# Performance work log

Measured on AMD Instinct MI355X. Metric: run time of the kernel, lower is better.

Reference implementation:

```python
import jax, jax.numpy as jnp
import numpy as np

HID = 512
HEADS = 8
HEAD_DIM = HID // HEADS
BS, SEQ = 4, 2048


def setup_inputs() -> dict:
    key = jax.random.key(0)
    ks = jax.random.split(key, 12)
    s = 0.02
    return {
        "query": jax.random.normal(ks[0], (BS, SEQ, HID), jnp.float32),
        "key": jax.random.normal(ks[1], (BS, SEQ, HID), jnp.float32),
        "value": jax.random.normal(ks[2], (BS, SEQ, HID), jnp.float32),
        "query_mask": jnp.ones((BS, SEQ), dtype=bool),
        "key_mask": jnp.ones((BS, SEQ), dtype=bool),
        "Wq": jax.random.normal(ks[3], (HID, HID), jnp.float32) * s,
        "bq": jnp.zeros((HID,), jnp.float32),
        "Wk": jax.random.normal(ks[4], (HID, HID), jnp.float32) * s,
        "bk": jnp.zeros((HID,), jnp.float32),
        "Wv": jax.random.normal(ks[5], (HID, HID), jnp.float32) * s,
        "bv": jnp.zeros((HID,), jnp.float32),
        "Wo": jax.random.normal(ks[6], (HID, HID), jnp.float32) * s,
        "bo": jnp.zeros((HID,), jnp.float32),
    }


def _mha(query, key, value, query_mask, key_mask, Wq, bq, Wk, bk, Wv, bv, Wo, bo):
    bs, q_len, _ = query.shape
    k_len = key.shape[1]
    scale = jnp.sqrt(jnp.asarray(HEAD_DIM, query.dtype))

    def proj(x, W, b):  # nn.Linear: x @ W^T + b, then split heads -> [b,h,s,d]
        y = jnp.einsum('bse,fe->bsf', x, W) + b
        return y.reshape(bs, -1, HEADS, HEAD_DIM).transpose(0, 2, 1, 3)

    q = proj(query, Wq, bq)
    k = proj(key, Wk, bk)
    v = proj(value, Wv, bv)

    energy = jnp.einsum('bhqd,bhkd->bhqk', q, k) / scale  # [b,h,q,k]
    neg = -jnp.finfo(energy.dtype).max

    pad_mask = query_mask[:, None, :, None] & key_mask[:, None, None, :]
    energy = jnp.where(pad_mask, energy, neg)

    # causal: mask positions where q_idx < k_idx
    causal = jnp.arange(q_len)[:, None] < jnp.arange(k_len)[None, :]
    energy = jnp.where(causal[None, None], neg, energy)

    attn = jax.nn.softmax(energy, axis=-1)  # dropout p=0.0 -> identity
    x = jnp.einsum('bhqk,bhkd->bhqd', attn, v)
    x = x.transpose(0, 2, 1, 3).reshape(bs, q_len, HID)
    return jnp.einsum('bse,fe->bsf', x, Wo) + bo


def reference(query, key, value, query_mask, key_mask, Wq, bq, Wk, bk, Wv, bv, Wo, bo):
    return _mha(query, key, value, query_mask, key_mask, Wq, bq, Wk, bk, Wv, bv, Wo, bo)
```

## Files before the change

kernel.cpp:

```cpp
#include <hip/hip_runtime.h>
#include <hip/hip_bf16.h>

#define DEVI __device__ __forceinline__

typedef __attribute__((ext_vector_type(4)))  float f32x4;
typedef __attribute__((ext_vector_type(16))) float f32x16;
typedef __attribute__((ext_vector_type(8)))  short bf16x8;

constexpr int BS    = 4;
constexpr int SEQ   = 2048;
constexpr int HID   = 512;
constexpr int HEADS = 8;
constexpr int HD    = 64;
constexpr int M     = BS * SEQ;

constexpr float QSCALE = 0.125f * 1.4426950408889634f;

DEVI ushort f2bf(float f) {
    union { float f; unsigned u; } a; a.f = f;
    unsigned r = a.u + 0x7fffu + ((a.u >> 16) & 1u);
    return (ushort)(r >> 16);
}

DEVI f32x4 mfma16(bf16x8 a, bf16x8 b, f32x4 c) {
    return __builtin_amdgcn_mfma_f32_16x16x32_bf16(a, b, c, 0, 0, 0);
}
DEVI f32x16 mfma32(bf16x8 a, bf16x8 b, f32x16 c) {
    return __builtin_amdgcn_mfma_f32_32x32x16_bf16(a, b, c, 0, 0, 0);
}

DEVI void gl_lds16(const ushort* g, ushort* l) {
    __builtin_amdgcn_global_load_lds(
        (const __attribute__((address_space(1))) void*)g,
        (__attribute__((address_space(3))) void*)l,
        16, 0, 0);
}

DEVI unsigned cvtpk(float lo, float hi) {
    unsigned r;
    asm("v_cvt_pk_bf16_f32 %0, %1, %2" : "=v"(r) : "v"(lo), "v"(hi));
    return r;
}

__global__ void cast_all(const float* __restrict__ q, const float* __restrict__ k,
                         const float* __restrict__ v,
                         const float* __restrict__ wq, const float* __restrict__ wk,
                         const float* __restrict__ wv, const float* __restrict__ wo,
                         ushort* __restrict__ oq, ushort* __restrict__ ok,
                         ushort* __restrict__ ov,
                         ushort* __restrict__ owq, ushort* __restrict__ owk,
                         ushort* __restrict__ owv, ushort* __restrict__ owo)
{
    const size_t NQ4 = (size_t)M * HID / 4;
    const size_t NW4 = (size_t)HID * HID / 4;
    const size_t total = 3 * NQ4 + 4 * NW4;
    for (size_t i = (size_t)blockIdx.x * blockDim.x + threadIdx.x; i < total;
         i += (size_t)gridDim.x * blockDim.x) {
        const float* src; ushort* dst; size_t j;
        if (i < 3 * NQ4) {
            size_t a = i / NQ4; j = i - a * NQ4;
            src = (a == 0) ? q : (a == 1) ? k : v;
            dst = (a == 0) ? oq : (a == 1) ? ok : ov;
        } else {
            size_t t = i - 3 * NQ4;
            size_t a = t / NW4; j = t - a * NW4;
            src = (a == 0) ? wq : (a == 1) ? wk : (a == 2) ? wv : wo;
            dst = (a == 0) ? owq : (a == 1) ? owk : (a == 2) ? owv : owo;
        }
        float4 f = ((const float4*)src)[j];
        ushort4 u;
        u.x = f2bf(f.x); u.y = f2bf(f.y); u.z = f2bf(f.z); u.w = f2bf(f.w);
        ((ushort4*)dst)[j] = u;
    }
}

DEVI void gemm_core(const ushort* __restrict__ A, const ushort* __restrict__ W,
                    const float* __restrict__ bias, void* __restrict__ out,
                    float scale, int mode, ushort* lA, ushort* lB)
{
    constexpr int BK = 32;
    const int tid  = threadIdx.x;
    const int lane = tid & 63, w = tid >> 6;
    const int wm = w >> 1, wn = w & 1;
    const int l15 = lane & 15, lg = lane >> 4;
    const int m0 = blockIdx.x * 64, n0 = blockIdx.y * 128;
    const int srow = tid >> 2, sc8 = (tid & 3) * 8;

    f32x4 acc[2][4];
    #pragma unroll
    for (int i = 0; i < 2; i++)
        #pragma unroll
        for (int n = 0; n < 4; n++) acc[i][n] = f32x4{0.f, 0.f, 0.f, 0.f};

    for (int k0 = 0; k0 < HID; k0 += BK) {
        gl_lds16(A + (size_t)(m0 + srow) * HID + k0 + sc8, lA + w * 512);
        gl_lds16(W + (size_t)(n0 + srow) * HID + k0 + sc8, lB + w * 512);
        gl_lds16(W + (size_t)(n0 + 64 + srow) * HID + k0 + sc8, lB + 2048 + w * 512);
        __syncthreads();

        bf16x8 af[2], bfr[4];
        #pragma unroll
        for (int i = 0; i < 2; i++)
            af[i] = *(const bf16x8*)(lA + (wm * 32 + i * 16 + l15) * BK + lg * 8);
        #pragma unroll
        for (int n = 0; n < 4; n++)
            bfr[n] = *(const bf16x8*)(lB + (wn * 64 + n * 16 + l15) * BK + lg * 8);
        #pragma unroll
        for (int i = 0; i < 2; i++)
            #pragma unroll
            for (int n = 0; n < 4; n++)
                acc[i][n] = mfma16(af[i], bfr[n], acc[i][n]);
        __syncthreads();
    }

    #pragma unroll
    for (int i = 0; i < 2; i++) {
        #pragma unroll
        for (int n = 0; n < 4; n++) {
            const int col = n0 + wn * 64 + n * 16 + l15;
            const float bb = bias[col];
            const int rbase = m0 + wm * 32 + i * 16 + lg * 4;
            #pragma unroll
            for (int jj = 0; jj < 4; jj++) {
                float v = (acc[i][n][jj] + bb) * scale;
                const int r = rbase + jj;
                if (mode == 3) {
                    ((float*)out)[(size_t)r * HID + col] = v;
                } else {
                    const int b = r >> 11, s = r & (SEQ - 1);
                    const int h = col >> 6, d = col & 63;
                    const int bh = b * HEADS + h;
                    const int t = s >> 5;
                    const ushort u = f2bf(v);
                    if (mode == 0) {
                        const int l31r = s & 31;
                        const int ds = d >> 4, hif = (d >> 3) & 1, jf = d & 7;
                        ((ushort*)out)[(((size_t)bh * 64 + t) * 4 + ds) * 512 +
                                       (hif * 32 + l31r) * 8 + jf] = u;
                    } else {
                        const int c = s & 31;
                        const int kvh = (c >> 4) & 1, hif = (c >> 2) & 1;
                        const int jf = (c & 3) + ((c >> 3) & 1) * 4;
                        const int dt = d >> 5, drow = d & 31;
                        ((ushort*)out)[(((size_t)bh * 64 + t) * 4 + dt * 2 + kvh) * 512 +
                                       (hif * 32 + drow) * 8 + jf] = u;
                    }
                }
            }
        }
    }
}

__global__ __launch_bounds__(256)
void gemm_qkv(const ushort* __restrict__ Xq, const ushort* __restrict__ Xk,
              const ushort* __restrict__ Xv,
              const ushort* __restrict__ Wq, const ushort* __restrict__ Wk,
              const ushort* __restrict__ Wv,
              const float* __restrict__ bq, const float* __restrict__ bk,
              const float* __restrict__ bv,
              ushort* __restrict__ Qf, ushort* __restrict__ Kf,
              ushort* __restrict__ Vf)
{
    __shared__ ushort lA[64 * 32];
    __shared__ ushort lB[128 * 32];
    const int z = blockIdx.z;
    const ushort* A = z == 0 ? Xq : z == 1 ? Xk : Xv;
    const ushort* W = z == 0 ? Wq : z == 1 ? Wk : Wv;
    const float* bias = z == 0 ? bq : z == 1 ? bk : bv;
    void* out = z == 0 ? (void*)Qf : z == 1 ? (void*)Kf : (void*)Vf;
    gemm_core(A, W, bias, out, z == 0 ? QSCALE : 1.0f, z == 2 ? 2 : 0, lA, lB);
}

__global__ __launch_bounds__(256)
void gemm_o(const ushort* __restrict__ ctx, const ushort* __restrict__ Wo,
            const float* __restrict__ bo, float* __restrict__ out)
{
    __shared__ ushort lA[64 * 32];
    __shared__ ushort lB[128 * 32];
    gemm_core(ctx, Wo, bo, out, 1.0f, 3, lA, lB);
}

__global__ __launch_bounds__(256)
void attn4(const ushort* __restrict__ Qf, const ushort* __restrict__ Kf,
           const ushort* __restrict__ Vf, ushort* __restrict__ ctx)
{
    __shared__ float part[4][2][16][64];
    __shared__ float pml[4][2][32];

    const int tid  = threadIdx.x;
    const int lane = tid & 63, w = tid >> 6;
    const int l31 = lane & 31, hi = lane >> 5;

    const int bid = blockIdx.x;
    const int bh  = bid & 31;
    const int qt  = 63 - (bid >> 5);
    const int qb  = qt * 32;

    const ushort* Qb = Qf + ((size_t)bh * 64 + qt) * 2048;
    const ushort* Kb = Kf + (size_t)bh * 64 * 2048;
    const ushort* Vb = Vf + (size_t)bh * 64 * 2048;

    bf16x8 qf[4];
    #pragma unroll
    for (int ds = 0; ds < 4; ds++)
        qf[ds] = *(const bf16x8*)(Qb + ds * 512 + lane * 8);

    f32x16 acc0 = {}, acc1 = {};
    float mrun = -3e38f, lrun = 0.f;

    bf16x8 kf[4] = {};
    if (w <= qt) {
        const ushort* kp = Kb + (size_t)w * 2048 + lane * 8;
        #pragma unroll
        for (int ds = 0; ds < 4; ds++)
            kf[ds] = *(const bf16x8*)(kp + ds * 512);
    }

    for (int t = w; t <= qt; t += 4) {
        const ushort* vp = Vb + (size_t)t * 2048 + lane * 8;
        const bf16x8 va00 = *(const bf16x8*)(vp);
        const bf16x8 va01 = *(const bf16x8*)(vp + 512);
        const bf16x8 va10 = *(const bf16x8*)(vp + 1024);
        const bf16x8 va11 = *(const bf16x8*)(vp + 1536);

        f32x16 s = {};
        #pragma unroll
        for (int ds = 0; ds < 4; ds++)
            s = mfma32(kf[ds], qf[ds], s);

        {
            const int tn = (t + 4 <= qt) ? t + 4 : t;
            const ushort* kp = Kb + (size_t)tn * 2048 + lane * 8;
            #pragma unroll
            for (int ds = 0; ds < 4; ds++)
                kf[ds] = *(const bf16x8*)(kp + ds * 512);
        }

        if (t == qt) {
            #pragma unroll
            for (int r = 0; r < 16; r++) {
                const int kvrow = (r & 3) + 8 * (r >> 2) + 4 * hi;
                s[r] = (kvrow > l31) ? -3e38f : s[r];
            }
        }

        float m8[8];
        #pragma unroll
        for (int r = 0; r < 8; r++) m8[r] = fmaxf(s[r], s[r + 8]);
        float m4a = fmaxf(m8[0], m8[1]), m4b = fmaxf(m8[2], m8[3]);
        float m4c = fmaxf(m8[4], m8[5]), m4d = fmaxf(m8[6], m8[7]);
        float pmax = fmaxf(fmaxf(m4a, m4b), fmaxf(m4c, m4d));
        pmax = fmaxf(pmax, __shfl_xor(pmax, 32));

        if (!__all(pmax <= mrun + 8.f)) {
            const float mnew = fmaxf(mrun, pmax);
            const float corr = __builtin_amdgcn_exp2f(mrun - mnew);
            lrun *= corr;
            #pragma unroll
            for (int r = 0; r < 16; r++) { acc0[r] *= corr; acc1[r] *= corr; }
            mrun = mnew;
        }

        float e[16];
        #pragma unroll
        for (int r = 0; r < 16; r++)
            e[r] = __builtin_amdgcn_exp2f(s[r] - mrun);
        float es0 = (e[0] + e[1]) + (e[2] + e[3]);
        float es1 = (e[4] + e[5]) + (e[6] + e[7]);
        float es2 = (e[8] + e[9]) + (e[10] + e[11]);
        float es3 = (e[12] + e[13]) + (e[14] + e[15]);
        float esum = (es0 + es1) + (es2 + es3);
        lrun += esum + __shfl_xor(esum, 32);

        union { unsigned u[4]; bf16x8 v; } pb0, pb1;
        pb0.u[0] = cvtpk(e[0],  e[1]);  pb0.u[1] = cvtpk(e[2],  e[3]);
        pb0.u[2] = cvtpk(e[4],  e[5]);  pb0.u[3] = cvtpk(e[6],  e[7]);
        pb1.u[0] = cvtpk(e[8],  e[9]);  pb1.u[1] = cvtpk(e[10], e[11]);
        pb1.u[2] = cvtpk(e[12], e[13]); pb1.u[3] = cvtpk(e[14], e[15]);

        acc0 = mfma32(va00, pb0.v, acc0);
        acc0 = mfma32(va01, pb1.v, acc0);
        acc1 = mfma32(va10, pb0.v, acc1);
        acc1 = mfma32(va11, pb1.v, acc1);
    }

    #pragma unroll
    for (int r = 0; r < 16; r++) {
        part[w][0][r][lane] = acc0[r];
        part[w][1][r][lane] = acc1[r];
    }
    if (hi == 0) { pml[w][0][l31] = mrun; pml[w][1][l31] = lrun; }
    __syncthreads();

    const float mm0 = pml[0][0][l31], ll0 = pml[0][1][l31];
    const float mm1 = pml[1][0][l31], ll1 = pml[1][1][l31];
    const float mm2 = pml[2][0][l31], ll2 = pml[2][1][l31];
    const float mm3 = pml[3][0][l31], ll3 = pml[3][1][l31];
    const float mstar = fmaxf(fmaxf(mm0, mm1), fmaxf(mm2, mm3));
    const float f0 = __builtin_amdgcn_exp2f(mm0 - mstar);
    const float f1 = __builtin_amdgcn_exp2f(mm1 - mstar);
    const float f2 = __builtin_amdgcn_exp2f(mm2 - mstar);
    const float f3 = __builtin_amdgcn_exp2f(mm3 - mstar);
    const float lstar = ll0 * f0 + ll1 * f1 + ll2 * f2 + ll3 * f3;
    const float inv = 1.f / lstar;

    const int b = bh >> 3, h = bh & 7;
    ushort* op = ctx + ((size_t)(b * SEQ + qb + l31)) * HID + h * HD;
    #pragma unroll
    for (int a = 0; a < 2; a++) {
        float v[4];
        #pragma unroll
        for (int j = 0; j < 4; j++) {
            const int r = 4 * w + j;
            v[j] = (part[0][a][r][lane] * f0 + part[1][a][r][lane] * f1 +
                    part[2][a][r][lane] * f2 + part[3][a][r][lane] * f3) * inv;
        }
        ushort4 o;
        o.x = f2bf(v[0]); o.y = f2bf(v[1]); o.z = f2bf(v[2]); o.w = f2bf(v[3]);
        *(ushort4*)(op + a * 32 + 8 * w + 4 * hi) = o;
    }
}

extern "C" void kernel_launch(void* const* d_in, const int* in_sizes, int n_in,
                              void* d_out, int out_size, void* d_ws, size_t ws_size,
                              hipStream_t stream) {
    const float* q  = (const float*)d_in[0];
    const float* k  = (const float*)d_in[1];
    const float* v  = (const float*)d_in[2];
    const float* Wq = (const float*)d_in[5];
    const float* bq = (const float*)d_in[6];
    const float* Wk = (const float*)d_in[7];
    const float* bk = (const float*)d_in[8];
    const float* Wv = (const float*)d_in[9];
    const float* bv = (const float*)d_in[10];
    const float* Wo = (const float*)d_in[11];
    const float* bo = (const float*)d_in[12];

    char* ws = (char*)d_ws;
    constexpr size_t XSZ = (size_t)M * HID * 2;
    constexpr size_t WSZ = (size_t)HID * HID * 2;
    ushort* Xq  = (ushort*)(ws);
    ushort* Xk  = (ushort*)(ws + XSZ);
    ushort* Xv  = (ushort*)(ws + 2 * XSZ);
    ushort* Wqb = (ushort*)(ws + 3 * XSZ);
    ushort* Wkb = (ushort*)(ws + 3 * XSZ + WSZ);
    ushort* Wvb = (ushort*)(ws + 3 * XSZ + 2 * WSZ);
    ushort* Wob = (ushort*)(ws + 3 * XSZ + 3 * WSZ);
    ushort* Qf  = (ushort*)(ws + 3 * XSZ + 4 * WSZ);
    ushort* Kf  = (ushort*)(ws + 4 * XSZ + 4 * WSZ);
    ushort* Vf  = (ushort*)(ws + 5 * XSZ + 4 * WSZ);
    ushort* ctx = (ushort*)(ws + 6 * XSZ + 4 * WSZ);

    cast_all<<<2048, 256, 0, stream>>>(q, k, v, Wq, Wk, Wv, Wo,
                                       Xq, Xk, Xv, Wqb, Wkb, Wvb, Wob);

    dim3 gqkv(M / 64, HID / 128, 3);
    gemm_qkv<<<gqkv, 256, 0, stream>>>(Xq, Xk, Xv, Wqb, Wkb, Wvb,
                                       bq, bk, bv, Qf, Kf, Vf);

    attn4<<<BS * HEADS * (SEQ / 32), 256, 0, stream>>>(Qf, Kf, Vf, ctx);

    dim3 go(M / 64, HID / 128);
    gemm_o<<<go, 256, 0, stream>>>(ctx, Wob, bo, (float*)d_out);
}
```

Before: 95.82 us.

## Fuse activation bf16 cast into QKV GEMM, enlarge M tile, prefetch V

The separate cast of the query/key/value activations is removed: the QKV GEMM now loads fp32 rows directly, converts them to bf16 in registers and writes them to LDS, so only the weights are cast up front. Both GEMMs move from 64x128 to 128x128 tiles, which doubles the accumulators per wave and halves the grid. The attention loop now prefetches the next tile's V fragments together with K into registers. This saves a full round trip of activations through global memory, at the cost of higher register pressure, fewer blocks and a synchronous fp32 load path in the GEMM.

```diff
diff --git a/kernel.cpp b/kernel.cpp
--- a/kernel.cpp
+++ b/kernel.cpp
@@ -42,39 +42,24 @@
     return r;
 }
 
-__global__ void cast_all(const float* __restrict__ q, const float* __restrict__ k,
-                         const float* __restrict__ v,
-                         const float* __restrict__ wq, const float* __restrict__ wk,
-                         const float* __restrict__ wv, const float* __restrict__ wo,
-                         ushort* __restrict__ oq, ushort* __restrict__ ok,
-                         ushort* __restrict__ ov,
-                         ushort* __restrict__ owq, ushort* __restrict__ owk,
-                         ushort* __restrict__ owv, ushort* __restrict__ owo)
-{
-    const size_t NQ4 = (size_t)M * HID / 4;
-    const size_t NW4 = (size_t)HID * HID / 4;
-    const size_t total = 3 * NQ4 + 4 * NW4;
-    for (size_t i = (size_t)blockIdx.x * blockDim.x + threadIdx.x; i < total;
-         i += (size_t)gridDim.x * blockDim.x) {
-        const float* src; ushort* dst; size_t j;
-        if (i < 3 * NQ4) {
-            size_t a = i / NQ4; j = i - a * NQ4;
-            src = (a == 0) ? q : (a == 1) ? k : v;
-            dst = (a == 0) ? oq : (a == 1) ? ok : ov;
-        } else {
-            size_t t = i - 3 * NQ4;
-            size_t a = t / NW4; j = t - a * NW4;
-            src = (a == 0) ? wq : (a == 1) ? wk : (a == 2) ? wv : wo;
-            dst = (a == 0) ? owq : (a == 1) ? owk : (a == 2) ? owv : owo;
-        }
-        float4 f = ((const float4*)src)[j];
-        ushort4 u;
-        u.x = f2bf(f.x); u.y = f2bf(f.y); u.z = f2bf(f.z); u.w = f2bf(f.w);
-        ((ushort4*)dst)[j] = u;
-    }
-}
-
-DEVI void gemm_core(const ushort* __restrict__ A, const ushort* __restrict__ W,
+__global__ void cast_w(const float* __restrict__ wq, const float* __restrict__ wk,
+                       const float* __restrict__ wv, const float* __restrict__ wo,
+                       ushort* __restrict__ oq, ushort* __restrict__ ok,
+                       ushort* __restrict__ ov, ushort* __restrict__ oo)
+{
+    const int NW4 = HID * HID / 4;
+    int i = blockIdx.x * blockDim.x + threadIdx.x;
+    const int a = i >> 16, j = i & (NW4 - 1);
+    const float* src = (a == 0) ? wq : (a == 1) ? wk : (a == 2) ? wv : wo;
+    ushort* dst = (a == 0) ? oq : (a == 1) ? ok : (a == 2) ? ov : oo;
+    float4 f = ((const float4*)src)[j];
+    ushort4 u;
+    u.x = f2bf(f.x); u.y = f2bf(f.y); u.z = f2bf(f.z); u.w = f2bf(f.w);
+    ((ushort4*)dst)[j] = u;
+}
+
+template<bool AF32>
+DEVI void gemm_core(const void* __restrict__ Ain, const ushort* __restrict__ W,
                     const float* __restrict__ bias, void* __restrict__ out,
                     float scale, int mode, ushort* lA, ushort* lB)
 {
@@ -83,30 +68,46 @@
     const int lane = tid & 63, w = tid >> 6;
     const int wm = w >> 1, wn = w & 1;
     const int l15 = lane & 15, lg = lane >> 4;
-    const int m0 = blockIdx.x * 64, n0 = blockIdx.y * 128;
+    const int m0 = blockIdx.x * 128, n0 = blockIdx.y * 128;
     const int srow = tid >> 2, sc8 = (tid & 3) * 8;
-
-    f32x4 acc[2][4];
-    #pragma unroll
-    for (int i = 0; i < 2; i++)
+    const int arow = tid >> 1, ach = (tid & 1) * 16;
+
+    f32x4 acc[4][4];
+    #pragma unroll
+    for (int i = 0; i < 4; i++)
         #pragma unroll
         for (int n = 0; n < 4; n++) acc[i][n] = f32x4{0.f, 0.f, 0.f, 0.f};
 
     for (int k0 = 0; k0 < HID; k0 += BK) {
-        gl_lds16(A + (size_t)(m0 + srow) * HID + k0 + sc8, lA + w * 512);
+        if constexpr (AF32) {
+            const float4* ap = (const float4*)((const float*)Ain +
+                                (size_t)(m0 + arow) * HID + k0 + ach);
+            const float4 a0 = ap[0], a1 = ap[1], a2 = ap[2], a3 = ap[3];
+            union { unsigned u[4]; bf16x8 v; } p0, p1;
+            p0.u[0] = cvtpk(a0.x, a0.y); p0.u[1] = cvtpk(a0.z, a0.w);
+            p0.u[2] = cvtpk(a1.x, a1.y); p0.u[3] = cvtpk(a1.z, a1.w);
+            p1.u[0] = cvtpk(a2.x, a2.y); p1.u[1] = cvtpk(a2.z, a2.w);
+            p1.u[2] = cvtpk(a3.x, a3.y); p1.u[3] = cvtpk(a3.z, a3.w);
+            *(bf16x8*)(lA + arow * 32 + ach)     = p0.v;
+            *(bf16x8*)(lA + arow * 32 + ach + 8) = p1.v;
+        } else {
+            const ushort* A = (const ushort*)Ain;
+            gl_lds16(A + (size_t)(m0 + srow) * HID + k0 + sc8, lA + w * 512);
+            gl_lds16(A + (size_t)(m0 + 64 + srow) * HID + k0 + sc8, lA + 2048 + w * 512);
+        }
         gl_lds16(W + (size_t)(n0 + srow) * HID + k0 + sc8, lB + w * 512);
         gl_lds16(W + (size_t)(n0 + 64 + srow) * HID + k0 + sc8, lB + 2048 + w * 512);
         __syncthreads();
 
-        bf16x8 af[2], bfr[4];
-        #pragma unroll
-        for (int i = 0; i < 2; i++)
-            af[i] = *(const bf16x8*)(lA + (wm * 32 + i * 16 + l15) * BK + lg * 8);
+        bf16x8 af[4], bfr[4];
+        #pragma unroll
+        for (int i = 0; i < 4; i++)
+            af[i] = *(const bf16x8*)(lA + (wm * 64 + i * 16 + l15) * BK + lg * 8);
         #pragma unroll
         for (int n = 0; n < 4; n++)
             bfr[n] = *(const bf16x8*)(lB + (wn * 64 + n * 16 + l15) * BK + lg * 8);
         #pragma unroll
-        for (int i = 0; i < 2; i++)
+        for (int i = 0; i < 4; i++)
             #pragma unroll
             for (int n = 0; n < 4; n++)
                 acc[i][n] = mfma16(af[i], bfr[n], acc[i][n]);
@@ -114,12 +115,12 @@
     }
 
     #pragma unroll
-    for (int i = 0; i < 2; i++) {
+    for (int i = 0; i < 4; i++) {
         #pragma unroll
         for (int n = 0; n < 4; n++) {
             const int col = n0 + wn * 64 + n * 16 + l15;
             const float bb = bias[col];
-            const int rbase = m0 + wm * 32 + i * 16 + lg * 4;
+            const int rbase = m0 + wm * 64 + i * 16 + lg * 4;
             #pragma unroll
             for (int jj = 0; jj < 4; jj++) {
                 float v = (acc[i][n][jj] + bb) * scale;
@@ -152,8 +153,8 @@
 }
 
 __global__ __launch_bounds__(256)
-void gemm_qkv(const ushort* __restrict__ Xq, const ushort* __restrict__ Xk,
-              const ushort* __restrict__ Xv,
+void gemm_qkv(const float* __restrict__ Xq, const float* __restrict__ Xk,
+              const float* __restrict__ Xv,
               const ushort* __restrict__ Wq, const ushort* __restrict__ Wk,
               const ushort* __restrict__ Wv,
               const float* __restrict__ bq, const float* __restrict__ bk,
@@ -161,27 +162,27 @@
               ushort* __restrict__ Qf, ushort* __restrict__ Kf,
               ushort* __restrict__ Vf)
 {
-    __shared__ ushort lA[64 * 32];
+    __shared__ ushort lA[128 * 32];
     __shared__ ushort lB[128 * 32];
     const int z = blockIdx.z;
-    const ushort* A = z == 0 ? Xq : z == 1 ? Xk : Xv;
+    const float* A = z == 0 ? Xq : z == 1 ? Xk : Xv;
     const ushort* W = z == 0 ? Wq : z == 1 ? Wk : Wv;
     const float* bias = z == 0 ? bq : z == 1 ? bk : bv;
     void* out = z == 0 ? (void*)Qf : z == 1 ? (void*)Kf : (void*)Vf;
-    gemm_core(A, W, bias, out, z == 0 ? QSCALE : 1.0f, z == 2 ? 2 : 0, lA, lB);
+    gemm_core<true>(A, W, bias, out, z == 0 ? QSCALE : 1.0f, z == 2 ? 2 : 0, lA, lB);
 }
 
 __global__ __launch_bounds__(256)
 void gemm_o(const ushort* __restrict__ ctx, const ushort* __restrict__ Wo,
             const float* __restrict__ bo, float* __restrict__ out)
 {
-    __shared__ ushort lA[64 * 32];
+    __shared__ ushort lA[128 * 32];
     __shared__ ushort lB[128 * 32];
-    gemm_core(ctx, Wo, bo, out, 1.0f, 3, lA, lB);
+    gemm_core<false>(ctx, Wo, bo, out, 1.0f, 3, lA, lB);
 }
 
 __global__ __launch_bounds__(256)
-void attn4(const ushort* __restrict__ Qf, const ushort* __restrict__ Kf,
+void attn5(const ushort* __restrict__ Qf, const ushort* __restrict__ Kf,
            const ushort* __restrict__ Vf, ushort* __restrict__ ctx)
 {
     __shared__ float part[4][2][16][64];
@@ -208,32 +209,33 @@
     f32x16 acc0 = {}, acc1 = {};
     float mrun = -3e38f, lrun = 0.f;
 
-    bf16x8 kf[4] = {};
+    bf16x8 kf[4] = {}, va[4] = {};
     if (w <= qt) {
         const ushort* kp = Kb + (size_t)w * 2048 + lane * 8;
-        #pragma unroll
-        for (int ds = 0; ds < 4; ds++)
+        const ushort* vp = Vb + (size_t)w * 2048 + lane * 8;
+        #pragma unroll
+        for (int ds = 0; ds < 4; ds++) {
             kf[ds] = *(const bf16x8*)(kp + ds * 512);
+            va[ds] = *(const bf16x8*)(vp + ds * 512);
+        }
     }
 
     for (int t = w; t <= qt; t += 4) {
-        const ushort* vp = Vb + (size_t)t * 2048 + lane * 8;
-        const bf16x8 va00 = *(const bf16x8*)(vp);
-        const bf16x8 va01 = *(const bf16x8*)(vp + 512);
-        const bf16x8 va10 = *(const bf16x8*)(vp + 1024);
-        const bf16x8 va11 = *(const bf16x8*)(vp + 1536);
-
         f32x16 s = {};
         #pragma unroll
         for (int ds = 0; ds < 4; ds++)
             s = mfma32(kf[ds], qf[ds], s);
 
+        bf16x8 kfn[4], van[4];
         {
             const int tn = (t + 4 <= qt) ? t + 4 : t;
             const ushort* kp = Kb + (size_t)tn * 2048 + lane * 8;
-            #pragma unroll
-            for (int ds = 0; ds < 4; ds++)
-                kf[ds] = *(const bf16x8*)(kp + ds * 512);
+            const ushort* vp = Vb + (size_t)tn * 2048 + lane * 8;
+            #pragma unroll
+            for (int ds = 0; ds < 4; ds++) {
+                kfn[ds] = *(const bf16x8*)(kp + ds * 512);
+                van[ds] = *(const bf16x8*)(vp + ds * 512);
+            }
         }
 
         if (t == qt) {
@@ -278,10 +280,13 @@
         pb1.u[0] = cvtpk(e[8],  e[9]);  pb1.u[1] = cvtpk(e[10], e[11]);
         pb1.u[2] = cvtpk(e[12], e[13]); pb1.u[3] = cvtpk(e[14], e[15]);
 
-        acc0 = mfma32(va00, pb0.v, acc0);
-        acc0 = mfma32(va01, pb1.v, acc0);
-        acc1 = mfma32(va10, pb0.v, acc1);
-        acc1 = mfma32(va11, pb1.v, acc1);
+        acc0 = mfma32(va[0], pb0.v, acc0);
+        acc0 = mfma32(va[1], pb1.v, acc0);
+        acc1 = mfma32(va[2], pb0.v, acc1);
+        acc1 = mfma32(va[3], pb1.v, acc1);
+
+        #pragma unroll
+        for (int ds = 0; ds < 4; ds++) { kf[ds] = kfn[ds]; va[ds] = van[ds]; }
     }
 
     #pragma unroll
@@ -339,27 +344,23 @@
     char* ws = (char*)d_ws;
     constexpr size_t XSZ = (size_t)M * HID * 2;
     constexpr size_t WSZ = (size_t)HID * HID * 2;
-    ushort* Xq  = (ushort*)(ws);
-    ushort* Xk  = (ushort*)(ws + XSZ);
-    ushort* Xv  = (ushort*)(ws + 2 * XSZ);
-    ushort* Wqb = (ushort*)(ws + 3 * XSZ);
-    ushort* Wkb = (ushort*)(ws + 3 * XSZ + WSZ);
-    ushort* Wvb = (ushort*)(ws + 3 * XSZ + 2 * WSZ);
-    ushort* Wob = (ushort*)(ws + 3 * XSZ + 3 * WSZ);
-    ushort* Qf  = (ushort*)(ws + 3 * XSZ + 4 * WSZ);
-    ushort* Kf  = (ushort*)(ws + 4 * XSZ + 4 * WSZ);
-    ushort* Vf  = (ushort*)(ws + 5 * XSZ + 4 * WSZ);
-    ushort* ctx = (ushort*)(ws + 6 * XSZ + 4 * WSZ);
-
-    cast_all<<<2048, 256, 0, stream>>>(q, k, v, Wq, Wk, Wv, Wo,
-                                       Xq, Xk, Xv, Wqb, Wkb, Wvb, Wob);
-
-    dim3 gqkv(M / 64, HID / 128, 3);
-    gemm_qkv<<<gqkv, 256, 0, stream>>>(Xq, Xk, Xv, Wqb, Wkb, Wvb,
+    ushort* Wqb = (ushort*)(ws);
+    ushort* Wkb = (ushort*)(ws + WSZ);
+    ushort* Wvb = (ushort*)(ws + 2 * WSZ);
+    ushort* Wob = (ushort*)(ws + 3 * WSZ);
+    ushort* Qf  = (ushort*)(ws + 4 * WSZ);
+    ushort* Kf  = (ushort*)(ws + 4 * WSZ + XSZ);
+    ushort* Vf  = (ushort*)(ws + 4 * WSZ + 2 * XSZ);
+    ushort* ctx = (ushort*)(ws + 4 * WSZ + 3 * XSZ);
+
+    cast_w<<<1024, 256, 0, stream>>>(Wq, Wk, Wv, Wo, Wqb, Wkb, Wvb, Wob);
+
+    dim3 gqkv(M / 128, HID / 128, 3);
+    gemm_qkv<<<gqkv, 256, 0, stream>>>(q, k, v, Wqb, Wkb, Wvb,
                                        bq, bk, bv, Qf, Kf, Vf);
 
-    attn4<<<BS * HEADS * (SEQ / 32), 256, 0, stream>>>(Qf, Kf, Vf, ctx);
-
-    dim3 go(M / 64, HID / 128);
+    attn5<<<BS * HEADS * (SEQ / 32), 256, 0, stream>>>(Qf, Kf, Vf, ctx);
+
+    dim3 go(M / 128, HID / 128);
     gemm_o<<<go, 256, 0, stream>>>(ctx, Wob, bo, (float*)d_out);
 }
```

Result: faster. 92.95 us (-3.0%).
